# Performance work log

Measured on AMD Instinct MI355X. Metric: run time of the kernel, lower is better.

## Reference

```python
import jax, jax.numpy as jnp
import numpy as np

EPS = 1e-8

def rms_norm(x, g):
    xf = x.astype(jnp.float32)
    ms = jnp.mean(xf * xf, axis=-1, keepdims=True)
    return (g * (xf * jax.lax.rsqrt(ms + EPS))).astype(x.dtype)

def setup_inputs() -> dict:
    key = jax.random.key(0)
    ks = jax.random.split(key, 10)
    B, S, D, H = 2, 2048, 1024, 16
    x = jax.random.normal(ks[0], (B, S, D), dtype=jnp.float32)
    p_bias = jax.random.normal(ks[1], (H, S, S), dtype=jnp.float32) * 0.02
    # additive causal mask [S, S]
    causal = jnp.tril(jnp.ones((S, S), dtype=bool))
    mask = jnp.where(causal, 0.0, -1e9).astype(jnp.float32)
    sd = 1.0 / np.sqrt(D)
    w_qkv = jax.random.normal(ks[2], (3 * D, D), dtype=jnp.float32) * sd
    w_u = jax.random.normal(ks[3], (D, D), dtype=jnp.float32) * sd
    g_ams = jnp.ones((D,), dtype=jnp.float32)
    w0 = jax.random.normal(ks[4], (D, D), dtype=jnp.float32) * sd
    w1 = jax.random.normal(ks[5], (2 * D, D), dtype=jnp.float32) * sd
    w3 = jax.random.normal(ks[6], (D, D), dtype=jnp.float32) * sd
    g_mffn = jnp.ones((D,), dtype=jnp.float32)
    return {"x": x, "p_bias": p_bias, "mask": mask, "w_qkv": w_qkv,
            "w_u": w_u, "g_ams": g_ams, "w0": w0, "w1": w1, "w3": w3,
            "g_mffn": g_mffn}

def reference(x, p_bias, mask, w_qkv, w_u, g_ams, w0, w1, w3, g_mffn):
    B, S, D = x.shape
    H = p_bias.shape[0]
    Dh = D // H
    scale = Dh ** -0.5
    # ---- AMS layer ----
    xn = rms_norm(x, g_ams)
    qkv = (xn @ w_qkv.T).reshape(B, S, 3, H, Dh)
    q, k, v = qkv[:, :, 0], qkv[:, :, 1], qkv[:, :, 2]  # [B,S,H,Dh]
    # scores: [B,H,S,S]
    score = jnp.einsum('bqhd,bkhd->bhqk', q, k) * scale
    score = score + p_bias[None] + mask[None, None]
    prob = jax.nn.silu(score)
    attn = jnp.einsum('bhqk,bkhd->bqhd', prob, v).reshape(B, S, D)
    u = jax.nn.silu(xn @ w_u.T)
    ams_out = attn * u
    # ---- MFFN layer ----
    o = ams_out @ w0.T + x
    on = rms_norm(o, g_mffn)
    x12 = on @ w1.T
    x1, x2 = jnp.split(x12, 2, axis=-1)
    hidden = jax.nn.silu(x1) * x2
    return hidden @ w3.T + o
```

## Files before the change

### kernel.cpp

```cpp
#include <hip/hip_runtime.h>
#include <hip/hip_bf16.h>
#include <cstdint>
#include <cstddef>

typedef __bf16 bf16x8 __attribute__((ext_vector_type(8)));
typedef float  f32x4  __attribute__((ext_vector_type(4)));
using u16 = unsigned short;
using u32 = unsigned int;

__device__ __forceinline__ float b2f(u16 u) {
  u32 v = ((u32)u) << 16;
  float f; __builtin_memcpy(&f, &v, 4); return f;
}
__device__ __forceinline__ u16 f2b(float f) {
  u32 v; __builtin_memcpy(&v, &f, 4);
  u32 r = v + 0x7fffu + ((v >> 16) & 1u);
  return (u16)(r >> 16);
}
__device__ __forceinline__ float silu(float x) {
  return x / (1.f + __expf(-x));
}
__device__ __forceinline__ f32x4 zero4() { f32x4 v = {0.f,0.f,0.f,0.f}; return v; }

typedef __attribute__((address_space(1))) const void* gas_ptr;
typedef __attribute__((address_space(3))) void*       las_ptr;
__device__ __forceinline__ void async_copy16(const void* g, void* l) {
  __builtin_amdgcn_global_load_lds((gas_ptr)g, (las_ptr)l, 16, 0, 0);
}

__global__ __launch_bounds__(256) void cvt_kernel(
    const float* __restrict__ wqkv, const float* __restrict__ wu,
    const float* __restrict__ w0,   const float* __restrict__ w1,
    const float* __restrict__ w3,
    u16* bqkv, u16* bu, u16* b0, u16* b1, u16* b3)
{
  const int blk = blockIdx.x;
  const float* src; u16* dst; int base;
  if      (blk < 3072) { src = wqkv; dst = bqkv; base = blk; }
  else if (blk < 4096) { src = wu;   dst = bu;   base = blk - 3072; }
  else if (blk < 5120) { src = w0;   dst = b0;   base = blk - 4096; }
  else if (blk < 7168) { src = w1;   dst = b1;   base = blk - 5120; }
  else                 { src = w3;   dst = b3;   base = blk - 7168; }
  const size_t i = (size_t)base * 1024 + threadIdx.x * 4;
  float4 v = *(const float4*)(src + i);
  uint2 o;
  o.x = (u32)f2b(v.x) | ((u32)f2b(v.y) << 16);
  o.y = (u32)f2b(v.z) | ((u32)f2b(v.w) << 16);
  *(uint2*)(dst + i) = o;
}

__global__ __launch_bounds__(256) void gemm_qkvu(
    const u16* __restrict__ A, const u16* __restrict__ Bw,
    u16* __restrict__ qkv_out, u16* __restrict__ u_out, int K)
{
  __shared__ u16 sA[128 * 32];
  __shared__ u16 sB[128 * 32];

  const int t    = threadIdx.x;
  const int wave = t >> 6, lane = t & 63;
  const int quad = lane >> 4, l16 = lane & 15;
  const int wm = wave >> 1, wn = wave & 1;

  const int nwg = gridDim.x * gridDim.y;
  const int bid = blockIdx.y * gridDim.x + blockIdx.x;
  const int v   = (bid & 7) * (nwg >> 3) + (bid >> 3);
  const int bx  = v % gridDim.x, by = v / gridDim.x;
  const int m0 = by * 128, n0 = bx * 128;

  const int arow = t >> 2, achunk = t & 3;
  const u16* gA = A  + (size_t)(m0 + arow) * K + achunk * 8;
  const u16* gB = Bw + (size_t)(n0 + arow) * K + achunk * 8;
  u16* lA = sA + t * 8;
  u16* lB = sB + t * 8;

  f32x4 acc[4][4];
#pragma unroll
  for (int i = 0; i < 4; i++)
#pragma unroll
    for (int j = 0; j < 4; j++) acc[i][j] = zero4();

  for (int kb = 0; kb < K; kb += 32) {
    async_copy16(gA + kb,                 lA);
    async_copy16(gA + kb + (size_t)64*K,  lA + 2048);
    async_copy16(gB + kb,                 lB);
    async_copy16(gB + kb + (size_t)64*K,  lB + 2048);
    __syncthreads();

    bf16x8 af[4], bfr[4];
#pragma unroll
    for (int mi = 0; mi < 4; mi++)
      af[mi]  = *(const bf16x8*)(sA + (wm*64 + mi*16 + l16)*32 + quad*8);
#pragma unroll
    for (int ni = 0; ni < 4; ni++)
      bfr[ni] = *(const bf16x8*)(sB + (wn*64 + ni*16 + l16)*32 + quad*8);
#pragma unroll
    for (int mi = 0; mi < 4; mi++)
#pragma unroll
      for (int ni = 0; ni < 4; ni++)
        acc[mi][ni] = __builtin_amdgcn_mfma_f32_16x16x32_bf16(af[mi], bfr[ni], acc[mi][ni], 0, 0, 0);
    __syncthreads();
  }

#pragma unroll
  for (int mi = 0; mi < 4; mi++) {
#pragma unroll
    for (int ni = 0; ni < 4; ni++) {
#pragma unroll
      for (int r = 0; r < 4; r++) {
        const int row = m0 + wm*64 + mi*16 + quad*4 + r;
        const int col = n0 + wn*64 + ni*16 + l16;
        float vv = acc[mi][ni][r];
        if (col < 3072) {
          qkv_out[(size_t)row * 3072 + col] = f2b(vv);
        } else {
          u_out[(size_t)row * 1024 + (col - 3072)] = f2b(silu(vv));
        }
      }
    }
  }
}

template<int EPI>
__global__ __launch_bounds__(256) void gemm64_bt(
    const u16* __restrict__ A, const u16* __restrict__ Bw,
    const float* __restrict__ res, void* __restrict__ Cp,
    int M, int N, int K)
{
  __shared__ u16 sA[128 * 32];
  __shared__ u16 sB[ 64 * 32];

  const int t    = threadIdx.x;
  const int wave = t >> 6, lane = t & 63;
  const int quad = lane >> 4, l16 = lane & 15;
  const int wm = wave >> 1, wn = wave & 1;

  const int nwg = gridDim.x * gridDim.y;
  const int bid = blockIdx.y * gridDim.x + blockIdx.x;
  const int v   = (bid & 7) * (nwg >> 3) + (bid >> 3);
  const int bx  = v & (gridDim.x - 1), by = v / gridDim.x;
  const int m0 = by * 128, n0 = bx * 64;

  const int arow = t >> 2, achunk = t & 3;
  const u16* gA = A  + (size_t)(m0 + arow) * K + achunk * 8;
  const u16* gB = Bw + (size_t)(n0 + arow) * K + achunk * 8;
  u16* lA = sA + t * 8;
  u16* lB = sB + t * 8;

  f32x4 acc[4][2];
#pragma unroll
  for (int i = 0; i < 4; i++) { acc[i][0] = zero4(); acc[i][1] = zero4(); }

  for (int kb = 0; kb < K; kb += 32) {
    async_copy16(gA + kb,                 lA);
    async_copy16(gA + kb + (size_t)64*K,  lA + 2048);
    async_copy16(gB + kb,                 lB);
    __syncthreads();

    bf16x8 af[4], bfr[2];
#pragma unroll
    for (int mi = 0; mi < 4; mi++)
      af[mi]  = *(const bf16x8*)(sA + (wm*64 + mi*16 + l16)*32 + quad*8);
#pragma unroll
    for (int ni = 0; ni < 2; ni++)
      bfr[ni] = *(const bf16x8*)(sB + (wn*32 + ni*16 + l16)*32 + quad*8);
#pragma unroll
    for (int mi = 0; mi < 4; mi++)
#pragma unroll
      for (int ni = 0; ni < 2; ni++)
        acc[mi][ni] = __builtin_amdgcn_mfma_f32_16x16x32_bf16(af[mi], bfr[ni], acc[mi][ni], 0, 0, 0);
    __syncthreads();
  }

#pragma unroll
  for (int mi = 0; mi < 4; mi++) {
#pragma unroll
    for (int ni = 0; ni < 2; ni++) {
#pragma unroll
      for (int r = 0; r < 4; r++) {
        const int row = m0 + wm*64 + mi*16 + quad*4 + r;
        const int col = n0 + wn*32 + ni*16 + l16;
        const size_t idx = (size_t)row * N + col;
        ((float*)Cp)[idx] = acc[mi][ni][r] + res[idx];
      }
    }
  }
}

__global__ __launch_bounds__(256) void gemm_glu(
    const u16* __restrict__ A, const u16* __restrict__ Bw,
    u16* __restrict__ hid, int K)
{
  __shared__ u16 sA [128 * 32];
  __shared__ u16 sB1[ 64 * 32];
  __shared__ u16 sB2[ 64 * 32];

  const int t    = threadIdx.x;
  const int wave = t >> 6, lane = t & 63;
  const int quad = lane >> 4, l16 = lane & 15;
  const int wm = wave >> 1, wn = wave & 1;

  const int nwg = gridDim.x * gridDim.y;
  const int bid = blockIdx.y * gridDim.x + blockIdx.x;
  const int v   = (bid & 7) * (nwg >> 3) + (bid >> 3);
  const int bx  = v & (gridDim.x - 1), by = v / gridDim.x;
  const int m0 = by * 128, n0 = bx * 64;

  const int arow = t >> 2, achunk = t & 3;
  const u16* gA  = A  + (size_t)(m0 + arow) * K + achunk * 8;
  const u16* gB1 = Bw + (size_t)(n0 + arow) * K + achunk * 8;
  const u16* gB2 = Bw + (size_t)(n0 + 1024 + arow) * K + achunk * 8;
  u16* lA  = sA  + t * 8;
  u16* lB1 = sB1 + t * 8;
  u16* lB2 = sB2 + t * 8;

  f32x4 acc1[4][2], acc2[4][2];
#pragma unroll
  for (int i = 0; i < 4; i++) {
    acc1[i][0] = zero4(); acc1[i][1] = zero4();
    acc2[i][0] = zero4(); acc2[i][1] = zero4();
  }

  for (int kb = 0; kb < K; kb += 32) {
    async_copy16(gA + kb,                 lA);
    async_copy16(gA + kb + (size_t)64*K,  lA + 2048);
    async_copy16(gB1 + kb,                lB1);
    async_copy16(gB2 + kb,                lB2);
    __syncthreads();

    bf16x8 af[4], b1f[2], b2f[2];
#pragma unroll
    for (int mi = 0; mi < 4; mi++)
      af[mi] = *(const bf16x8*)(sA + (wm*64 + mi*16 + l16)*32 + quad*8);
#pragma unroll
    for (int ni = 0; ni < 2; ni++) {
      b1f[ni] = *(const bf16x8*)(sB1 + (wn*32 + ni*16 + l16)*32 + quad*8);
      b2f[ni] = *(const bf16x8*)(sB2 + (wn*32 + ni*16 + l16)*32 + quad*8);
    }
#pragma unroll
    for (int mi = 0; mi < 4; mi++)
#pragma unroll
      for (int ni = 0; ni < 2; ni++) {
        acc1[mi][ni] = __builtin_amdgcn_mfma_f32_16x16x32_bf16(af[mi], b1f[ni], acc1[mi][ni], 0, 0, 0);
        acc2[mi][ni] = __builtin_amdgcn_mfma_f32_16x16x32_bf16(af[mi], b2f[ni], acc2[mi][ni], 0, 0, 0);
      }
    __syncthreads();
  }

#pragma unroll
  for (int mi = 0; mi < 4; mi++) {
#pragma unroll
    for (int ni = 0; ni < 2; ni++) {
#pragma unroll
      for (int r = 0; r < 4; r++) {
        const int row = m0 + wm*64 + mi*16 + quad*4 + r;
        const int col = n0 + wn*32 + ni*16 + l16;
        hid[(size_t)row * 1024 + col] = f2b(silu(acc1[mi][ni][r]) * acc2[mi][ni][r]);
      }
    }
  }
}

__global__ __launch_bounds__(256) void vtrans_kernel(
    const u16* __restrict__ qkv, u16* __restrict__ vt)
{
  __shared__ u16 tile[64][72];
  const int st = blockIdx.x, bh = blockIdx.y;
  const int b = bh >> 4, h = bh & 15;
  const int t = threadIdx.x;
#pragma unroll
  for (int i = 0; i < 2; i++) {
    const int c = i * 256 + t;
    const int row = c >> 3, cc = c & 7;
    uint4 v = *(const uint4*)(qkv + (size_t)(b*2048 + st*64 + row)*3072 + 2048 + h*64 + cc*8);
    *(uint4*)(&tile[row][cc*8]) = v;
  }
  __syncthreads();
#pragma unroll
  for (int i = 0; i < 2; i++) {
    const int c = i * 256 + t;
    const int dh = c >> 3, cc = c & 7;
    u16 tmp[8];
#pragma unroll
    for (int j = 0; j < 8; j++) tmp[j] = tile[cc*8 + j][dh];
    *(uint4*)(vt + ((size_t)bh*64 + dh)*2048 + st*64 + cc*8) = *(uint4*)tmp;
  }
}

__global__ __launch_bounds__(1024) void attn_kernel(
    const u16* __restrict__ qkv,
    const u16* __restrict__ vt,
    const float* __restrict__ p_bias,
    const u16* __restrict__ ub,
    u16* __restrict__ am_out)
{
  constexpr int S = 2048, D3 = 3072;
  __shared__ u16 sQ [128 * 64];
  __shared__ u16 sK [128 * 64];
  __shared__ u16 sVt[ 64 * 128];
  __shared__ u16 sP [128 * 128];

  const int t    = threadIdx.x;
  const int wave = t >> 6, lane = t & 63;
  const int quad = lane >> 4, l16 = lane & 15;
  const int p  = blockIdx.x & 7, bh = blockIdx.x >> 3;
  const int b  = bh >> 4, h = bh & 15;
  const int wsq = wave & 3, wsk = wave >> 2;
  const int wpq = wave & 3, wpd = wave >> 2;
  const float scale = 0.125f;

  const int srow8 = lane >> 3, sc8 = lane & 7;
  const int srow16 = lane >> 4, sc16 = lane & 15;

#pragma unroll 1
  for (int sel = 0; sel < 2; sel++) {
    const int qt = sel ? 15 - p : p;
    const int q0 = qt * 128;

    __syncthreads();
    {
      const int row = wave * 8 + srow8;
      const int gc  = sc8 ^ (row & 7);
      async_copy16(qkv + (size_t)(b*S + q0 + row)*D3 + h*64 + gc*8,
                   sQ + wave*512 + lane*8);
    }

    f32x4 oacc[2];
    oacc[0] = zero4(); oacc[1] = zero4();

    for (int kt = 0; kt <= qt; kt++) {
      const int k0 = kt * 128;
      __syncthreads();
      {
        const int row = wave * 8 + srow8;
        const int gc  = sc8 ^ (row & 7);
        async_copy16(qkv + (size_t)(b*S + k0 + row)*D3 + 1024 + h*64 + gc*8,
                     sK + wave*512 + lane*8);
        const int vrow = wave * 4 + srow16;
        const int vgc  = sc16 ^ (vrow & 15);
        async_copy16(vt + ((size_t)bh*64 + vrow)*2048 + k0 + vgc*8,
                     sVt + wave*512 + lane*8);
      }
      __syncthreads();

      float bias[2][2][4];
#pragma unroll
      for (int mi = 0; mi < 2; mi++)
#pragma unroll
        for (int ni = 0; ni < 2; ni++)
#pragma unroll
          for (int r = 0; r < 4; r++) {
            const int q = wsq*32 + mi*16 + quad*4 + r;
            const int k = wsk*32 + ni*16 + l16;
            bias[mi][ni][r] = p_bias[((size_t)h*S + q0 + q)*S + k0 + k];
          }

      bf16x8 aq[2][2], bk[2][2];
#pragma unroll
      for (int mi = 0; mi < 2; mi++)
#pragma unroll
        for (int kk = 0; kk < 2; kk++) {
          const int row = wsq*32 + mi*16 + l16;
          const int phys = (quad + kk*4) ^ (row & 7);
          aq[mi][kk] = *(const bf16x8*)(sQ + row*64 + phys*8);
        }
#pragma unroll
      for (int ni = 0; ni < 2; ni++)
#pragma unroll
        for (int kk = 0; kk < 2; kk++) {
          const int row = wsk*32 + ni*16 + l16;
          const int phys = (quad + kk*4) ^ (row & 7);
          bk[ni][kk] = *(const bf16x8*)(sK + row*64 + phys*8);
        }

      f32x4 sacc[2][2];
#pragma unroll
      for (int mi = 0; mi < 2; mi++)
#pragma unroll
        for (int ni = 0; ni < 2; ni++) {
          f32x4 s = zero4();
          s = __builtin_amdgcn_mfma_f32_16x16x32_bf16(aq[mi][0], bk[ni][0], s, 0, 0, 0);
          s = __builtin_amdgcn_mfma_f32_16x16x32_bf16(aq[mi][1], bk[ni][1], s, 0, 0, 0);
          sacc[mi][ni] = s;
        }

#pragma unroll
      for (int mi = 0; mi < 2; mi++)
#pragma unroll
        for (int ni = 0; ni < 2; ni++)
#pragma unroll
          for (int r = 0; r < 4; r++) {
            const int q = wsq*32 + mi*16 + quad*4 + r;
            const int k = wsk*32 + ni*16 + l16;
            const int qi = q0 + q, ki = k0 + k;
            float vv = sacc[mi][ni][r] * scale + bias[mi][ni][r];
            vv = (ki <= qi) ? silu(vv) : 0.f;
            const int pc = (k >> 3) ^ (q & 15);
            sP[q*128 + pc*8 + (k & 7)] = f2b(vv);
          }
      __syncthreads();

#pragma unroll
      for (int kk = 0; kk < 4; kk++) {
        bf16x8 ap[2], bv;
#pragma unroll
        for (int mi = 0; mi < 2; mi++) {
          const int row = wpq*32 + mi*16 + l16;
          const int phys = (quad + kk*4) ^ (row & 15);
          ap[mi] = *(const bf16x8*)(sP + row*128 + phys*8);
        }
        {
          const int row = wpd*16 + l16;
          const int phys = (quad + kk*4) ^ (row & 15);
          bv = *(const bf16x8*)(&sVt[row*128 + phys*8]);
        }
#pragma unroll
        for (int mi = 0; mi < 2; mi++)
          oacc[mi] = __builtin_amdgcn_mfma_f32_16x16x32_bf16(ap[mi], bv, oacc[mi], 0, 0, 0);
      }
    }

#pragma unroll
    for (int mi = 0; mi < 2; mi++)
#pragma unroll
      for (int r = 0; r < 4; r++) {
        const int q  = wpq*32 + mi*16 + quad*4 + r;
        const int dh = wpd*16 + l16;
        const size_t oidx = (size_t)(b*S + q0 + q)*1024 + h*64 + dh;
        am_out[oidx] = f2b(oacc[mi][r] * b2f(ub[oidx]));
      }
  }
}

__global__ __launch_bounds__(256) void rmsnorm_kernel(
    const float* __restrict__ x, const float* __restrict__ g, u16* __restrict__ out)
{
  const int row = blockIdx.x, t = threadIdx.x;
  const int wave = t >> 6, lane = t & 63;
  const size_t base = (size_t)row * 1024;
  float v[4];
#pragma unroll
  for (int i = 0; i < 4; i++) v[i] = x[base + i * 256 + t];
  float ss = v[0]*v[0] + v[1]*v[1] + v[2]*v[2] + v[3]*v[3];
#pragma unroll
  for (int off = 32; off; off >>= 1) ss += __shfl_down(ss, off);
  __shared__ float red[4];
  if (lane == 0) red[wave] = ss;
  __syncthreads();
  const float r = rsqrtf((red[0] + red[1] + red[2] + red[3]) * (1.f / 1024.f) + 1e-8f);
#pragma unroll
  for (int i = 0; i < 4; i++) {
    const int j = i * 256 + t;
    out[base + j] = f2b(g[j] * v[i] * r);
  }
}

extern "C" void kernel_launch(void* const* d_in, const int* in_sizes, int n_in,
                              void* d_out, int out_size, void* d_ws, size_t ws_size,
                              hipStream_t stream)
{
  const float* x      = (const float*)d_in[0];
  const float* pbias  = (const float*)d_in[1];
  const float* w_qkv  = (const float*)d_in[3];
  const float* w_u    = (const float*)d_in[4];
  const float* g_ams  = (const float*)d_in[5];
  const float* w0     = (const float*)d_in[6];
  const float* w1     = (const float*)d_in[7];
  const float* w3     = (const float*)d_in[8];
  const float* g_mffn = (const float*)d_in[9];

  constexpr int M = 4096, D = 1024;
  char* ws = (char*)d_ws;
  u16*   xn    = (u16*)ws;
  u16*   qkv   = (u16*)(ws + (8u  << 20));
  u16*   ubuf  = (u16*)(ws + (32u << 20));
  u16*   am    = (u16*)(ws + (40u << 20));
  float* obuf  = (float*)(ws + (48u << 20));
  u16*   vt    = (u16*)(ws + (48u << 20));
  u16*   bqkv  = (u16*)(ws + (64u << 20));
  u16*   bu    = (u16*)(ws + (70u << 20));
  u16*   b0    = (u16*)(ws + (72u << 20));
  u16*   b1    = (u16*)(ws + (74u << 20));
  u16*   b3    = (u16*)(ws + (78u << 20));

  cvt_kernel<<<8192, 256, 0, stream>>>(w_qkv, w_u, w0, w1, w3, bqkv, bu, b0, b1, b3);
  rmsnorm_kernel<<<M, 256, 0, stream>>>(x, g_ams, xn);
  gemm_qkvu<<<dim3(32, 32), 256, 0, stream>>>(xn, bqkv, qkv, ubuf, D);
  vtrans_kernel<<<dim3(32, 32), 256, 0, stream>>>(qkv, vt);
  attn_kernel<<<256, 1024, 0, stream>>>(qkv, vt, pbias, ubuf, am);
  gemm64_bt<2><<<dim3(16, 32), 256, 0, stream>>>(am, b0, x, obuf, M, D, D);
  rmsnorm_kernel<<<M, 256, 0, stream>>>(obuf, g_mffn, ubuf);
  gemm_glu<<<dim3(16, 32), 256, 0, stream>>>(ubuf, b1, am, D);
  gemm64_bt<3><<<dim3(16, 32), 256, 0, stream>>>(am, b3, obuf, (float*)d_out, M, D, D);
}
```

Measured before the change: 606.4 us.

## Restructure attention to one q-tile per 512-thread block, heaviest tiles first

```diff
diff --git a/kernel.cpp b/kernel.cpp
--- a/kernel.cpp
+++ b/kernel.cpp
@@ -286,7 +286,7 @@
   }
 }
 
-__global__ __launch_bounds__(1024) void attn_kernel(
+__global__ __launch_bounds__(512, 4) void attn_kernel(
     const u16* __restrict__ qkv,
     const u16* __restrict__ vt,
     const float* __restrict__ p_bias,
@@ -302,133 +302,122 @@
   const int t    = threadIdx.x;
   const int wave = t >> 6, lane = t & 63;
   const int quad = lane >> 4, l16 = lane & 15;
-  const int p  = blockIdx.x & 7, bh = blockIdx.x >> 3;
-  const int b  = bh >> 4, h = bh & 15;
+  const int bid = blockIdx.x;
+  const int qt  = 15 - (bid >> 5);
+  const int bh  = bid & 31;
+  const int b   = bh >> 4, h = bh & 15;
+  const int q0  = qt * 128;
   const int wsq = wave & 3, wsk = wave >> 2;
   const int wpq = wave & 3, wpd = wave >> 2;
   const float scale = 0.125f;
 
-  const int srow8 = lane >> 3, sc8 = lane & 7;
-  const int srow16 = lane >> 4, sc16 = lane & 15;
-
-#pragma unroll 1
-  for (int sel = 0; sel < 2; sel++) {
-    const int qt = sel ? 15 - p : p;
-    const int q0 = qt * 128;
-
-    __syncthreads();
-    {
-      const int row = wave * 8 + srow8;
-      const int gc  = sc8 ^ (row & 7);
-      async_copy16(qkv + (size_t)(b*S + q0 + row)*D3 + h*64 + gc*8,
-                   sQ + wave*512 + lane*8);
+  const int srow = t >> 3, sc = t & 7;
+  const int sgc  = sc ^ (srow & 7);
+  const int vrow = t >> 4, vc = t & 15;
+  const int vgc  = vc ^ (vrow & 15);
+
+  const u16* gQ = qkv + (size_t)(b*S + q0 + srow)*D3 + h*64 + sgc*8;
+  const u16* gK = qkv + (size_t)(b*S + srow)*D3 + 1024 + h*64 + sgc*8;
+  const u16* gV = vt  + ((size_t)bh*64 + vrow)*2048 + vgc*8;
+
+  async_copy16(gQ,                      sQ + t*8);
+  async_copy16(gQ + (size_t)64*D3,      sQ + 4096 + t*8);
+
+  f32x4 oacc[2][2];
+  oacc[0][0] = zero4(); oacc[0][1] = zero4();
+  oacc[1][0] = zero4(); oacc[1][1] = zero4();
+
+  for (int kt = 0; kt <= qt; kt++) {
+    const int k0 = kt * 128;
+    __syncthreads();
+    async_copy16(gK + (size_t)k0*D3,                 sK + t*8);
+    async_copy16(gK + (size_t)(k0 + 64)*D3,          sK + 4096 + t*8);
+    async_copy16(gV + k0,                            sVt + t*8);
+    async_copy16(gV + (size_t)32*2048 + k0,          sVt + 4096 + t*8);
+    __syncthreads();
+
+    bf16x8 aq[2][2], bk[4][2];
+#pragma unroll
+    for (int mi = 0; mi < 2; mi++)
+#pragma unroll
+      for (int kk = 0; kk < 2; kk++) {
+        const int row = wsq*32 + mi*16 + l16;
+        const int phys = (quad + kk*4) ^ (row & 7);
+        aq[mi][kk] = *(const bf16x8*)(sQ + row*64 + phys*8);
+      }
+#pragma unroll
+    for (int ni = 0; ni < 4; ni++)
+#pragma unroll
+      for (int kk = 0; kk < 2; kk++) {
+        const int row = wsk*64 + ni*16 + l16;
+        const int phys = (quad + kk*4) ^ (row & 7);
+        bk[ni][kk] = *(const bf16x8*)(sK + row*64 + phys*8);
+      }
+
+    f32x4 sacc[2][4];
+#pragma unroll
+    for (int mi = 0; mi < 2; mi++)
+#pragma unroll
+      for (int ni = 0; ni < 4; ni++) {
+        f32x4 s = zero4();
+        s = __builtin_amdgcn_mfma_f32_16x16x32_bf16(aq[mi][0], bk[ni][0], s, 0, 0, 0);
+        s = __builtin_amdgcn_mfma_f32_16x16x32_bf16(aq[mi][1], bk[ni][1], s, 0, 0, 0);
+        sacc[mi][ni] = s;
+      }
+
+#pragma unroll
+    for (int mi = 0; mi < 2; mi++)
+#pragma unroll
+      for (int ni = 0; ni < 4; ni++) {
+        const int q_b = wsq*32 + mi*16 + quad*4;
+        const int k   = wsk*64 + ni*16 + l16;
+        const float* bp = p_bias + ((size_t)h*S + q0 + q_b)*S + k0 + k;
+#pragma unroll
+        for (int r = 0; r < 4; r++) {
+          const int q  = q_b + r;
+          const int qi = q0 + q, ki = k0 + k;
+          float vv = sacc[mi][ni][r] * scale + bp[(size_t)r*S];
+          vv = (ki <= qi) ? silu(vv) : 0.f;
+          const int pc = (k >> 3) ^ (q & 15);
+          sP[q*128 + pc*8 + (k & 7)] = f2b(vv);
+        }
+      }
+    __syncthreads();
+
+#pragma unroll
+    for (int kk = 0; kk < 4; kk++) {
+      bf16x8 ap[2], bv[2];
+#pragma unroll
+      for (int mi = 0; mi < 2; mi++) {
+        const int row = wpq*32 + mi*16 + l16;
+        const int phys = (quad + kk*4) ^ (row & 15);
+        ap[mi] = *(const bf16x8*)(sP + row*128 + phys*8);
+      }
+#pragma unroll
+      for (int ni = 0; ni < 2; ni++) {
+        const int row = wpd*32 + ni*16 + l16;
+        const int phys = (quad + kk*4) ^ (row & 15);
+        bv[ni] = *(const bf16x8*)(sVt + row*128 + phys*8);
+      }
+#pragma unroll
+      for (int mi = 0; mi < 2; mi++)
+#pragma unroll
+        for (int ni = 0; ni < 2; ni++)
+          oacc[mi][ni] = __builtin_amdgcn_mfma_f32_16x16x32_bf16(ap[mi], bv[ni], oacc[mi][ni], 0, 0, 0);
     }
-
-    f32x4 oacc[2];
-    oacc[0] = zero4(); oacc[1] = zero4();
-
-    for (int kt = 0; kt <= qt; kt++) {
-      const int k0 = kt * 128;
-      __syncthreads();
-      {
-        const int row = wave * 8 + srow8;
-        const int gc  = sc8 ^ (row & 7);
-        async_copy16(qkv + (size_t)(b*S + k0 + row)*D3 + 1024 + h*64 + gc*8,
-                     sK + wave*512 + lane*8);
-        const int vrow = wave * 4 + srow16;
-        const int vgc  = sc16 ^ (vrow & 15);
-        async_copy16(vt + ((size_t)bh*64 + vrow)*2048 + k0 + vgc*8,
-                     sVt + wave*512 + lane*8);
-      }
-      __syncthreads();
-
-      float bias[2][2][4];
-#pragma unroll
-      for (int mi = 0; mi < 2; mi++)
-#pragma unroll
-        for (int ni = 0; ni < 2; ni++)
-#pragma unroll
-          for (int r = 0; r < 4; r++) {
-            const int q = wsq*32 + mi*16 + quad*4 + r;
-            const int k = wsk*32 + ni*16 + l16;
-            bias[mi][ni][r] = p_bias[((size_t)h*S + q0 + q)*S + k0 + k];
-          }
-
-      bf16x8 aq[2][2], bk[2][2];
-#pragma unroll
-      for (int mi = 0; mi < 2; mi++)
-#pragma unroll
-        for (int kk = 0; kk < 2; kk++) {
-          const int row = wsq*32 + mi*16 + l16;
-          const int phys = (quad + kk*4) ^ (row & 7);
-          aq[mi][kk] = *(const bf16x8*)(sQ + row*64 + phys*8);
-        }
-#pragma unroll
-      for (int ni = 0; ni < 2; ni++)
-#pragma unroll
-        for (int kk = 0; kk < 2; kk++) {
-          const int row = wsk*32 + ni*16 + l16;
-          const int phys = (quad + kk*4) ^ (row & 7);
-          bk[ni][kk] = *(const bf16x8*)(sK + row*64 + phys*8);
-        }
-
-      f32x4 sacc[2][2];
-#pragma unroll
-      for (int mi = 0; mi < 2; mi++)
-#pragma unroll
-        for (int ni = 0; ni < 2; ni++) {
-          f32x4 s = zero4();
-          s = __builtin_amdgcn_mfma_f32_16x16x32_bf16(aq[mi][0], bk[ni][0], s, 0, 0, 0);
-          s = __builtin_amdgcn_mfma_f32_16x16x32_bf16(aq[mi][1], bk[ni][1], s, 0, 0, 0);
-          sacc[mi][ni] = s;
-        }
-
-#pragma unroll
-      for (int mi = 0; mi < 2; mi++)
-#pragma unroll
-        for (int ni = 0; ni < 2; ni++)
-#pragma unroll
-          for (int r = 0; r < 4; r++) {
-            const int q = wsq*32 + mi*16 + quad*4 + r;
-            const int k = wsk*32 + ni*16 + l16;
-            const int qi = q0 + q, ki = k0 + k;
-            float vv = sacc[mi][ni][r] * scale + bias[mi][ni][r];
-            vv = (ki <= qi) ? silu(vv) : 0.f;
-            const int pc = (k >> 3) ^ (q & 15);
-            sP[q*128 + pc*8 + (k & 7)] = f2b(vv);
-          }
-      __syncthreads();
-
-#pragma unroll
-      for (int kk = 0; kk < 4; kk++) {
-        bf16x8 ap[2], bv;
-#pragma unroll
-        for (int mi = 0; mi < 2; mi++) {
-          const int row = wpq*32 + mi*16 + l16;
-          const int phys = (quad + kk*4) ^ (row & 15);
-          ap[mi] = *(const bf16x8*)(sP + row*128 + phys*8);
-        }
-        {
-          const int row = wpd*16 + l16;
-          const int phys = (quad + kk*4) ^ (row & 15);
-          bv = *(const bf16x8*)(&sVt[row*128 + phys*8]);
-        }
-#pragma unroll
-        for (int mi = 0; mi < 2; mi++)
-          oacc[mi] = __builtin_amdgcn_mfma_f32_16x16x32_bf16(ap[mi], bv, oacc[mi], 0, 0, 0);
-      }
-    }
-
-#pragma unroll
-    for (int mi = 0; mi < 2; mi++)
+  }
+
+#pragma unroll
+  for (int mi = 0; mi < 2; mi++)
+#pragma unroll
+    for (int ni = 0; ni < 2; ni++)
 #pragma unroll
       for (int r = 0; r < 4; r++) {
         const int q  = wpq*32 + mi*16 + quad*4 + r;
-        const int dh = wpd*16 + l16;
+        const int dh = wpd*32 + ni*16 + l16;
         const size_t oidx = (size_t)(b*S + q0 + q)*1024 + h*64 + dh;
-        am_out[oidx] = f2b(oacc[mi][r] * b2f(ub[oidx]));
-      }
-  }
+        am_out[oidx] = f2b(oacc[mi][ni][r] * b2f(ub[oidx]));
+      }
 }
 
 __global__ __launch_bounds__(256) void rmsnorm_kernel(
@@ -486,7 +475,7 @@
   rmsnorm_kernel<<<M, 256, 0, stream>>>(x, g_ams, xn);
   gemm_qkvu<<<dim3(32, 32), 256, 0, stream>>>(xn, bqkv, qkv, ubuf, D);
   vtrans_kernel<<<dim3(32, 32), 256, 0, stream>>>(qkv, vt);
-  attn_kernel<<<256, 1024, 0, stream>>>(qkv, vt, pbias, ubuf, am);
+  attn_kernel<<<512, 512, 0, stream>>>(qkv, vt, pbias, ubuf, am);
   gemm64_bt<2><<<dim3(16, 32), 256, 0, stream>>>(am, b0, x, obuf, M, D, D);
   rmsnorm_kernel<<<M, 256, 0, stream>>>(obuf, g_mffn, ubuf);
   gemm_glu<<<dim3(16, 32), 256, 0, stream>>>(ubuf, b1, am, D);
```

New measurement: 842.7 us. +39.0%, slower.
